# Performance work log

Measured on AMD Instinct MI355X. Metric: run time of the kernel, lower is better.

Reference implementation:

```python
import jax, jax.numpy as jnp
import numpy as np

B, N, E, D, F_IN, EDGE_DIM, VN = 128, 500, 1048576, 128, 5, 2, 10
NEG_FEAT = 0.01   # torch F.leaky_relu default
NEG_ATT = 0.2     # GAT attention slope


def _gat_layer(h_in, src, dst, edge_attr, W, b, a_src, a_dst, a_edge, We, n_nodes):
    # Edge-feature GAT conv: per-edge attention over (src, dst, edge) then
    # softmax-normalized scatter-aggregate onto destination nodes.
    h = h_in @ W                                  # [N, d]
    e = edge_attr @ We                            # [E, d] projected edge features
    logits = jax.nn.leaky_relu((h @ a_src)[src] + (h @ a_dst)[dst] + e @ a_edge,
                               negative_slope=NEG_ATT)    # [E]
    # segment softmax over incoming edges of each dst node
    m = jax.ops.segment_max(logits, dst, num_segments=n_nodes)
    ex = jnp.exp(logits - m[dst])
    denom = jax.ops.segment_sum(ex, dst, num_segments=n_nodes)
    alpha = ex / (denom[dst] + 1e-16)             # [E]
    msg = h[src] + e                              # [E, d]
    out = jax.ops.segment_sum(alpha[:, None] * msg, dst, num_segments=n_nodes)
    return out + b


def setup_inputs() -> dict:
    key = jax.random.key(0)
    ks = jax.random.split(key, 20)
    s = 0.05
    return {
        'x': jax.random.normal(ks[0], (B * N, F_IN), jnp.float32),
        'edge_index': jax.random.randint(ks[1], (2, E), 0, B * N, jnp.int64 if jax.config.jax_enable_x64 else jnp.int32).astype(jnp.int32),
        'edge_attr': jax.random.uniform(ks[2], (E, EDGE_DIM), jnp.float32),
        'curr_v_node_id': jax.random.randint(ks[3], (B,), 0, VN).astype(jnp.int32),
        'v_graph_embedding': jax.random.normal(ks[4], (B, D), jnp.float32),
        'v_node_dense_embeddings': jax.random.normal(ks[5], (B, VN, D), jnp.float32),
        'p_W': jax.random.normal(ks[6], (F_IN, D), jnp.float32) * s,
        'p_b': jnp.zeros((D,), jnp.float32),
        'Ws': jax.random.normal(ks[7], (4, D, D), jnp.float32) * s,
        'bs': jnp.zeros((4, D), jnp.float32),
        'a_srcs': jax.random.normal(ks[8], (4, D), jnp.float32) * s,
        'a_dsts': jax.random.normal(ks[9], (4, D), jnp.float32) * s,
        'a_edges': jax.random.normal(ks[10], (4, D), jnp.float32) * s,
        'Wes': jax.random.normal(ks[11], (4, EDGE_DIM, D), jnp.float32) * s,
        'W5': jax.random.normal(ks[12], (D, 1), jnp.float32) * s,
        'b5': jnp.zeros((1,), jnp.float32),
        'a_src5': jax.random.normal(ks[13], (1,), jnp.float32) * s,
        'a_dst5': jax.random.normal(ks[14], (1,), jnp.float32) * s,
        'a_edge5': jax.random.normal(ks[15], (1,), jnp.float32) * s,
        'We5': jax.random.normal(ks[16], (EDGE_DIM, 1), jnp.float32) * s,
    }


def reference(x, edge_index, edge_attr, curr_v_node_id, v_graph_embedding,
              v_node_dense_embeddings, p_W, p_b, Ws, bs, a_srcs, a_dsts,
              a_edges, Wes, W5, b5, a_src5, a_dst5, a_edge5, We5):
    n_nodes = x.shape[0]
    src, dst = edge_index[0], edge_index[1]
    # gather current v-node embedding: [B, D]
    curr_emb = v_node_dense_embeddings[jnp.arange(B), curr_v_node_id]
    # linear + leaky_relu then broadcast-add of graph/node context
    h = jax.nn.leaky_relu(x @ p_W + p_b, negative_slope=NEG_FEAT)  # [B*N, D]
    h = h.reshape(B, N, D) + v_graph_embedding[:, None, :] + curr_emb[:, None, :]
    h = h.reshape(B * N, D)
    # 4 hidden edge-feature GAT layers (128 -> 128) with leaky_relu
    for l in range(4):
        h = _gat_layer(h, src, dst, edge_attr, Ws[l], bs[l], a_srcs[l],
                       a_dsts[l], a_edges[l], Wes[l], n_nodes)
        h = jax.nn.leaky_relu(h, negative_slope=NEG_FEAT)
    # output layer (128 -> 1), no activation
    h = _gat_layer(h, src, dst, edge_attr, W5, b5, a_src5, a_dst5, a_edge5,
                   We5, n_nodes)                    # [B*N, 1]
    return h.reshape(B, N)
```

## Files before the change

### kernel.cpp

```cpp
#include <hip/hip_runtime.h>
#include <hip/hip_bf16.h>

#define BB   128
#define NN   500
#define NV   64000
#define EE   1048576
#define DD   128
#define FIN  5
#define VNN  10
#define NBUK 250
#define BCAP 8192

typedef unsigned int   uint32;
typedef unsigned short u16b;
typedef __attribute__((ext_vector_type(8))) short short8;
typedef __attribute__((ext_vector_type(4))) float float4v;
typedef __attribute__((ext_vector_type(2))) float float2v;

#define P_ASRC  0
#define P_ADST  512
#define P_WE    1024
#define P_BIAS  2048
#define P_W5    2560
#define P_CVEC  2688
#define P_SC5   2700
#define P_ASD   2816
#define P_TOT   3840

static __device__ __forceinline__ float bf2f(__hip_bfloat16 v) { return __bfloat162float(v); }
static __device__ __forceinline__ float lo2f(uint32 u) { return __uint_as_float(u << 16); }
static __device__ __forceinline__ float hi2f(uint32 u) { return __uint_as_float(u & 0xFFFF0000u); }
static __device__ __forceinline__ uint32 f2bf_bits(float f) {
    uint32 u = __float_as_uint(f);
    return (u + 0x7FFFu + ((u >> 16) & 1u)) >> 16;
}
static __device__ __forceinline__ uint32 pack2(float a, float b) {
    return (f2bf_bits(a) & 0xFFFFu) | (f2bf_bits(b) << 16);
}
static __device__ __forceinline__ float2v unp2(uint32 u) {
    float2v r; r.x = lo2f(u); r.y = hi2f(u); return r;
}
static __device__ __forceinline__ float2v fma2(float2v a, float2v b, float2v c) {
#if __has_builtin(__builtin_elementwise_fma)
    return __builtin_elementwise_fma(a, b, c);
#else
    float2v r; r.x = fmaf(a.x, b.x, c.x); r.y = fmaf(a.y, b.y, c.y); return r;
#endif
}
static __device__ __forceinline__ float2v fma2s(float2v a, float w, float2v c) {
    float2v ww = {w, w};
    return fma2(a, ww, c);
}
static __device__ __forceinline__ float2v shfl_xor2(float2v v, int o) {
    double d; __builtin_memcpy(&d, &v, 8);
    d = __shfl_xor(d, o, 64);
    float2v r; __builtin_memcpy(&r, &d, 8);
    return r;
}
static __device__ __forceinline__ float2v lrelu2(float2v x, float slope) {
    float2v z = {0.f, 0.f};
#if __has_builtin(__builtin_elementwise_max)
    float2v p = __builtin_elementwise_max(x, z);
    float2v q = __builtin_elementwise_min(x, z);
#else
    float2v p; p.x = fmaxf(x.x, 0.f); p.y = fmaxf(x.y, 0.f);
    float2v q; q.x = fminf(x.x, 0.f); q.y = fminf(x.y, 0.f);
#endif
    float2v s = {slope, slope};
    return fma2(q, s, p);
}
static __device__ __forceinline__ float ldf(const void* p, int i, int flag) {
    return flag ? ((const float*)p)[i] : bf2f(((const __hip_bfloat16*)p)[i]);
}

__global__ void sniff_kernel(const unsigned short* __restrict__ p16, int* __restrict__ FLAG) {
    __shared__ int sHigh, sZero;
    if (threadIdx.x == 0) { sHigh = 0; sZero = 0; }
    __syncthreads();
    unsigned short v = p16[2 * threadIdx.x];
    if (v >= 0x8000u) atomicOr(&sHigh, 1);
    if (v == 0)       atomicAdd(&sZero, 1);
    __syncthreads();
    if (threadIdx.x == 0) FLAG[0] = (sHigh || sZero >= 128) ? 1 : 0;
}

__global__ void zero_out_kernel(void* __restrict__ out, const int* __restrict__ FLAG, float tag) {
    int i = blockIdx.x * blockDim.x + threadIdx.x;
    if (i >= NV) return;
    float v = (i == 0) ? tag : 0.f;
    if (FLAG[0]) ((float*)out)[i] = v;
    else         ((u16b*)out)[i] = (u16b)f2bf_bits(v);
}

__global__ void prep_kernel(const void* __restrict__ Wes, const void* __restrict__ aeg,
                            const void* __restrict__ We5, const void* __restrict__ ae5,
                            const void* __restrict__ asr, const void* __restrict__ ads,
                            const void* __restrict__ bs, const void* __restrict__ W5,
                            const void* __restrict__ b5, const void* __restrict__ as5,
                            const void* __restrict__ ad5, const int* __restrict__ FLAG,
                            float* __restrict__ PAR) {
    const int flag = FLAG[0];
    if (blockIdx.x == 0) {
        for (int i = threadIdx.x; i < 512; i += 256) PAR[P_ASRC + i] = ldf(asr, i, flag);
    } else if (blockIdx.x == 1) {
        for (int i = threadIdx.x; i < 512; i += 256) PAR[P_ADST + i] = ldf(ads, i, flag);
    } else if (blockIdx.x == 2) {
        for (int i = threadIdx.x; i < 1024; i += 256) PAR[P_WE + i] = ldf(Wes, i, flag);
    } else if (blockIdx.x == 3) {
        for (int i = threadIdx.x; i < 512; i += 256) PAR[P_BIAS + i] = ldf(bs, i, flag);
    } else if (blockIdx.x == 4) {
        int tid = threadIdx.x;
        if (tid < 128) {
            PAR[P_W5 + tid] = ldf(W5, tid, flag);
        } else if (tid < 136) {
            int l = (tid - 128) >> 1, r = (tid - 128) & 1;
            float s = 0.f;
            for (int ch = 0; ch < DD; ++ch)
                s += ldf(Wes, l * 256 + r * DD + ch, flag) * ldf(aeg, l * DD + ch, flag);
            PAR[P_CVEC + l * 2 + r] = s;
        } else if (tid == 136) {
            float ae = ldf(ae5, 0, flag);
            float w0 = ldf(We5, 0, flag), w1 = ldf(We5, 1, flag);
            PAR[P_CVEC + 8] = w0 * ae; PAR[P_CVEC + 9] = w1 * ae;
            PAR[P_CVEC + 10] = w0;     PAR[P_CVEC + 11] = w1;
            PAR[P_SC5 + 0] = ldf(b5, 0, flag);
            PAR[P_SC5 + 1] = ldf(as5, 0, flag);
            PAR[P_SC5 + 2] = ldf(ad5, 0, flag);
        }
    } else if (blockIdx.x == 5) {
        for (int i = threadIdx.x; i < 512; i += 256) {
            int l = i >> 7, c = i & 127;
            PAR[P_ASD + l * 256 + c * 2]     = ldf(asr, l * DD + c, flag);
            PAR[P_ASD + l * 256 + c * 2 + 1] = ldf(ads, l * DD + c, flag);
        }
    }
}

__global__ __launch_bounds__(256) void prepack_kernel(const void* __restrict__ Ws,
                                                      const int* __restrict__ FLAG,
                                                      u16b* __restrict__ WB) {
    const int flag = FLAG[0];
    int t = blockIdx.x * 256 + threadIdx.x;
    int lane = t & 63;
    int frag = t >> 6;
    int nchunk = frag & 7, kblk = (frag >> 3) & 3, l = frag >> 5;
    int n = nchunk * 16 + (lane & 15);
    int kbase = kblk * 32 + (lane >> 4) * 8;
#pragma unroll
    for (int j = 0; j < 8; ++j) {
        int idx = l * 16384 + (kbase + j) * 128 + n;
        u16b bits = flag ? (u16b)f2bf_bits(((const float*)Ws)[idx])
                         : ((const u16b*)Ws)[idx];
        WB[(size_t)t * 8 + j] = bits;
    }
}

__global__ __launch_bounds__(256) void proj_kernel(
        const void* __restrict__ x, const void* __restrict__ pW,
        const void* __restrict__ pb, const int* __restrict__ curr,
        const void* __restrict__ vge, const void* __restrict__ vnd,
        const int* __restrict__ FLAG, uint32* __restrict__ H) {
    const int flag = FLAG[0];
    const int n = blockIdx.x * 4 + (threadIdx.x >> 6);
    const int lane = threadIdx.x & 63;
    const int b = n / NN;
    int cv = curr[b]; if ((unsigned)cv >= VNN) cv = 0;
    float xv[FIN];
#pragma unroll
    for (int k = 0; k < FIN; ++k) xv[k] = ldf(x, n * FIN + k, flag);
    const int ch = lane * 2;
    float s0 = ldf(pb, ch, flag), s1 = ldf(pb, ch + 1, flag);
#pragma unroll
    for (int k = 0; k < FIN; ++k) {
        s0 = fmaf(xv[k], ldf(pW, k * DD + ch, flag), s0);
        s1 = fmaf(xv[k], ldf(pW, k * DD + ch + 1, flag), s1);
    }
    s0 = (s0 > 0.f) ? s0 : 0.01f * s0;
    s1 = (s1 > 0.f) ? s1 : 0.01f * s1;
    s0 += ldf(vge, b * DD + ch, flag) + ldf(vnd, (b * VNN + cv) * DD + ch, flag);
    s1 += ldf(vge, b * DD + ch + 1, flag) + ldf(vnd, (b * VNN + cv) * DD + ch + 1, flag);
    H[(size_t)n * 64 + lane] = pack2(s0, s1);
}

__global__ void init_kernel(int* __restrict__ gcur, int* __restrict__ counts) {
    int t = blockIdx.x * 256 + threadIdx.x;
    if (t < NBUK) gcur[t] = t * BCAP;
    if (t < 512) counts[NV + t] = 0;
}

__global__ __launch_bounds__(256) void bucketize_kernel(
        const int* __restrict__ src, const int* __restrict__ dst,
        const void* __restrict__ eaP, const int* __restrict__ FLAG,
        int* __restrict__ gcur, uint32* __restrict__ bukx, uint32* __restrict__ buky) {
    __shared__ int cnt[256];
    __shared__ int cur[256];
    const int flag = FLAG[0];
    const int t = threadIdx.x;
    const int e0 = blockIdx.x * 4096;
    cnt[t] = 0;
    __syncthreads();
    int d[16];
#pragma unroll
    for (int i = 0; i < 16; ++i) {
        d[i] = dst[e0 + i * 256 + t];
        if ((unsigned)d[i] >= NV) d[i] = -1;
        if (d[i] >= 0) atomicAdd(&cnt[d[i] >> 8], 1);
    }
    __syncthreads();
    if (t < NBUK) {
        int c = cnt[t];
        cur[t] = c ? atomicAdd(&gcur[t], c) : 0;
    }
    __syncthreads();
#pragma unroll
    for (int i = 0; i < 16; ++i) {
        if (d[i] < 0) continue;
        int e = e0 + i * 256 + t;
        int b = d[i] >> 8;
        int s = src[e];
        if ((unsigned)s >= NV) s = 0;
        uint32 eb;
        if (flag) { float2 v = ((const float2*)eaP)[e]; eb = pack2(v.x, v.y); }
        else      eb = ((const uint32*)eaP)[e];
        int p = atomicAdd(&cur[b], 1);
        if (p < (b + 1) * BCAP) {
            bukx[p] = (uint32)((s & 0xFFFF) | ((d[i] & 255) << 16));
            buky[p] = eb;
        }
    }
}

__global__ __launch_bounds__(256) void bcount_kernel(
        const uint32* __restrict__ bukx, const int* __restrict__ gcur,
        int* __restrict__ counts) {
    __shared__ int c[256];
    const int b = blockIdx.x, t = threadIdx.x;
    c[t] = 0;
    __syncthreads();
    const int base = b * BCAP;
    int cnt = gcur[b] - base;
    if (cnt > BCAP) cnt = BCAP;
    for (int i = t; i < cnt; i += 256)
        atomicAdd(&c[(bukx[base + i] >> 16) & 255], 1);
    __syncthreads();
    counts[b * 256 + t] = c[t];
}

__global__ __launch_bounds__(256) void scan1_kernel(const int* __restrict__ counts,
                                                    int* __restrict__ row_ptr,
                                                    int* __restrict__ partials) {
    __shared__ int sdata[256];
    int tid = threadIdx.x;
    int4 v = ((const int4*)counts)[blockIdx.x * 256 + tid];
    int sum = v.x + v.y + v.z + v.w;
    sdata[tid] = sum;
    __syncthreads();
    int acc = sum;
    for (int off = 1; off < 256; off <<= 1) {
        int t = (tid >= off) ? sdata[tid - off] : 0;
        __syncthreads();
        acc += t;
        sdata[tid] = acc;
        __syncthreads();
    }
    int excl = acc - sum;
    int base = blockIdx.x * 1024 + tid * 4;
    int run = excl;
    if (base + 0 <= NV) row_ptr[base + 0] = run; run += v.x;
    if (base + 1 <= NV) row_ptr[base + 1] = run; run += v.y;
    if (base + 2 <= NV) row_ptr[base + 2] = run; run += v.z;
    if (base + 3 <= NV) row_ptr[base + 3] = run;
    if (tid == 255) partials[blockIdx.x] = acc;
}

__global__ __launch_bounds__(64) void scan2_kernel(const int* __restrict__ partials,
                                                   int* __restrict__ boff, int nb) {
    int lane = threadIdx.x;
    int v = (lane < nb) ? partials[lane] : 0;
    int orig = v;
#pragma unroll
    for (int off = 1; off < 64; off <<= 1) {
        int t = __shfl_up(v, off, 64);
        if (lane >= off) v += t;
    }
    boff[lane] = v - orig;
}

__global__ __launch_bounds__(256) void scan3_kernel(int* __restrict__ row_ptr,
                                                    const int* __restrict__ boff) {
    int add = boff[blockIdx.x];
    int base = blockIdx.x * 1024 + threadIdx.x * 4;
#pragma unroll
    for (int j = 0; j < 4; ++j) {
        int i = base + j;
        if (i <= NV) row_ptr[i] += add;
    }
}

__global__ __launch_bounds__(256) void bscatter_kernel(
        const uint32* __restrict__ bukx, const uint32* __restrict__ buky,
        const int* __restrict__ gcur, const int* __restrict__ row_ptr,
        uint2* __restrict__ csr2) {
    __shared__ int cur[256];
    const int b = blockIdx.x, t = threadIdx.x;
    cur[t] = row_ptr[b * 256 + t];
    __syncthreads();
    const int base = b * BCAP;
    int cnt = gcur[b] - base;
    if (cnt > BCAP) cnt = BCAP;
    for (int i = t; i < cnt; i += 256) {
        uint32 x = bukx[base + i];
        uint32 y = buky[base + i];
        int p = atomicAdd(&cur[(x >> 16) & 255], 1);
        csr2[p] = make_uint2(x & 0xFFFFu, y);
    }
}

__global__ __launch_bounds__(256) void gemm_kernel(
        const uint32* __restrict__ Hu, const u16b* __restrict__ WBl,
        const float* __restrict__ ASDl, uint32* __restrict__ HWu,
        float* __restrict__ ssrc, float* __restrict__ sdst) {
    __shared__ float hs[64 * 129];
    const int tid = threadIdx.x;
    const int lane = tid & 63;
    const int wave = tid >> 6;
    const int quad = lane >> 4;
    const int n0 = blockIdx.x * 64;
    const int m = n0 + wave * 16 + (lane & 15);

    const u16b* hrow = (const u16b*)Hu + (size_t)m * 128;
    short8 a0 = *(const short8*)(hrow + 0  + quad * 8);
    short8 a1 = *(const short8*)(hrow + 32 + quad * 8);
    short8 a2 = *(const short8*)(hrow + 64 + quad * 8);
    short8 a3 = *(const short8*)(hrow + 96 + quad * 8);

    const float2v* asd = (const float2v*)ASDl;
    float2v psd[4];
#pragma unroll
    for (int r = 0; r < 4; ++r) { psd[r].x = 0.f; psd[r].y = 0.f; }

#pragma unroll
    for (int nt = 0; nt < 8; ++nt) {
        const u16b* bbase = WBl + ((size_t)nt * 512 + lane * 8);
        short8 b0 = *(const short8*)(bbase + 0 * 4096);
        short8 b1 = *(const short8*)(bbase + 1 * 4096);
        short8 b2 = *(const short8*)(bbase + 2 * 4096);
        short8 b3 = *(const short8*)(bbase + 3 * 4096);
        float4v acc = {0.f, 0.f, 0.f, 0.f};
        acc = __builtin_amdgcn_mfma_f32_16x16x32_bf16(a0, b0, acc, 0, 0, 0);
        acc = __builtin_amdgcn_mfma_f32_16x16x32_bf16(a1, b1, acc, 0, 0, 0);
        acc = __builtin_amdgcn_mfma_f32_16x16x32_bf16(a2, b2, acc, 0, 0, 0);
        acc = __builtin_amdgcn_mfma_f32_16x16x32_bf16(a3, b3, acc, 0, 0, 0);
        float2v av = asd[nt * 16 + (lane & 15)];
#pragma unroll
        for (int r = 0; r < 4; ++r) {
            hs[(wave * 16 + quad * 4 + r) * 129 + nt * 16 + (lane & 15)] = acc[r];
            psd[r] = fma2s(av, acc[r], psd[r]);
        }
    }
#pragma unroll
    for (int r = 0; r < 4; ++r) {
#pragma unroll
        for (int o = 1; o < 16; o <<= 1) {
            float2v other = shfl_xor2(psd[r], o);
            psd[r].x += other.x; psd[r].y += other.y;
        }
    }
    if ((lane & 15) == 0) {
#pragma unroll
        for (int r = 0; r < 4; ++r) {
            int row = n0 + wave * 16 + quad * 4 + r;
            ssrc[row] = psd[r].x;
            sdst[row] = psd[r].y;
        }
    }
    __syncthreads();

#pragma unroll
    for (int i = 0; i < 4; ++i) {
        int flat = i * 2048 + tid * 8;
        int n = flat >> 7, c = flat & 127;
        const float* p = hs + n * 129 + c;
        uint4 v;
        v.x = pack2(p[0], p[1]); v.y = pack2(p[2], p[3]);
        v.z = pack2(p[4], p[5]); v.w = pack2(p[6], p[7]);
        *(uint4*)(HWu + (size_t)(n0 + n) * 64 + c / 2) = v;
    }
}

__global__ __launch_bounds__(256, 4) void fused_kernel(
        const uint32* __restrict__ HWin, const float* __restrict__ ssrc,
        const float* __restrict__ sdst, const uint2* __restrict__ csr2,
        const int* __restrict__ row_ptr, const float* __restrict__ PAR,
        int layer, const u16b* __restrict__ WBn, const float* __restrict__ ASDn,
        uint32* __restrict__ HWout, float* __restrict__ ssrc_o,
        float* __restrict__ sdst_o, float* __restrict__ hw5out, int wantw5) {
    __shared__ uint32 Hlds[64 * 68];
    __shared__ float exs[4][64];
    const int tid = threadIdx.x;
    const int lane = tid & 63;
    const int wid = tid >> 6;
    const int n0 = blockIdx.x * 64;
    const float c0 = PAR[P_CVEC + 2 * layer], c1 = PAR[P_CVEC + 2 * layer + 1];
    const int ch = lane * 2;
    const float* WEl = PAR + P_WE + layer * 256;
    const float* Bl  = PAR + P_BIAS + layer * DD;
    const float2v we0 = *(const float2v*)(WEl + ch);
    const float2v we1 = *(const float2v*)(WEl + DD + ch);
    const float2v bl  = *(const float2v*)(Bl + ch);
    float w50 = 0.f, w51 = 0.f;
    if (wantw5) { w50 = PAR[P_W5 + ch]; w51 = PAR[P_W5 + ch + 1]; }

    for (int i = 0; i < 16; ++i) {
        const int n = n0 + wid * 16 + i;
        const int begin = __builtin_amdgcn_readfirstlane(row_ptr[n]);
        const int deg   = __builtin_amdgcn_readfirstlane(row_ptr[n + 1]) - begin;
        const float sd = sdst[n];

        int   sv = 0;
        uint32 eb = 0;
        if (lane < deg) {
            uint2 se = csr2[begin + lane];
            sv = (int)se.x;
            eb = se.y;
        }
        const float ssv = ssrc[sv];

        const int dmain = (deg < 64) ? deg : 64;
        const int npad  = (dmain + 15) & ~15;

        uint32 hA[16], hB[16];
#pragma unroll
        for (int q = 0; q < 16; ++q) {
            int s = __builtin_amdgcn_readlane(sv, q);
            hA[q] = HWin[(s << 6) + lane];
        }
        if (npad > 16) {
#pragma unroll
            for (int q = 0; q < 16; ++q) {
                int s = __builtin_amdgcn_readlane(sv, 16 + q);
                hB[q] = HWin[(s << 6) + lane];
            }
        }

        float ex = 0.f;
        if (lane < deg) {
            float L = fmaf(hi2f(eb), c1, fmaf(lo2f(eb), c0, ssv + sd));
            L = (L > 0.f) ? L : 0.2f * L;
            ex = __expf(fminf(L, 60.f));
        }
        exs[wid][lane] = ex;

        float2v acc2 = {0.f, 0.f};
        const float* wp = &exs[wid][0];
#pragma unroll
        for (int q0 = 0; q0 < 16; q0 += 4) {
            float4 w4 = *(const float4*)(wp + q0);
            acc2 = fma2s(unp2(hA[q0 + 0]), w4.x, acc2);
            acc2 = fma2s(unp2(hA[q0 + 1]), w4.y, acc2);
            acc2 = fma2s(unp2(hA[q0 + 2]), w4.z, acc2);
            acc2 = fma2s(unp2(hA[q0 + 3]), w4.w, acc2);
        }
        if (npad > 16) {
#pragma unroll
            for (int q0 = 16; q0 < 32; q0 += 4) {
                float4 w4 = *(const float4*)(wp + q0);
                acc2 = fma2s(unp2(hB[q0 - 16]), w4.x, acc2);
                acc2 = fma2s(unp2(hB[q0 - 15]), w4.y, acc2);
                acc2 = fma2s(unp2(hB[q0 - 14]), w4.z, acc2);
                acc2 = fma2s(unp2(hB[q0 - 13]), w4.w, acc2);
            }
        }
        for (int j = 32; j < dmain; ++j) {
            int s = __builtin_amdgcn_readlane(sv, j);
            float w = wp[j];
            acc2 = fma2s(unp2(HWin[(s << 6) + lane]), w, acc2);
        }

        float dsum = ex;
        float2v sxy = unp2(eb);
        sxy.x *= ex; sxy.y *= ex;
        for (int j0 = 64; j0 < deg; j0 += 64) {
            int j = j0 + lane;
            if (j < deg) {
                uint2 se2 = csr2[begin + j];
                float L2 = fmaf(hi2f(se2.y), c1, fmaf(lo2f(se2.y), c0, ssrc[se2.x] + sd));
                L2 = (L2 > 0.f) ? L2 : 0.2f * L2;
                float x2 = __expf(fminf(L2, 60.f));
                dsum += x2;
                sxy = fma2s(unp2(se2.y), x2, sxy);
            }
        }
#pragma unroll
        for (int o = 32; o; o >>= 1) {
            dsum += __shfl_xor(dsum, o, 64);
            float2v other = shfl_xor2(sxy, o);
            sxy.x += other.x; sxy.y += other.y;
        }

        for (int jj = 64; jj < deg; ++jj) {
            uint2 se2 = csr2[begin + jj];
            float L2 = fmaf(hi2f(se2.y), c1, fmaf(lo2f(se2.y), c0, ssrc[se2.x] + sd));
            L2 = (L2 > 0.f) ? L2 : 0.2f * L2;
            float x2 = __expf(fminf(L2, 60.f));
            acc2 = fma2s(unp2(HWin[(size_t)se2.x * 64 + lane]), x2, acc2);
        }

        const float inv = __builtin_amdgcn_rcpf(dsum + 1e-16f);
        float2v t2 = fma2s(we1, sxy.y, fma2s(we0, sxy.x, acc2));
        float2v o2 = fma2s(t2, inv, bl);
        o2 = lrelu2(o2, 0.01f);

        if (wantw5) {
            float p = o2.x * w50 + o2.y * w51;
#pragma unroll
            for (int o = 32; o; o >>= 1) p += __shfl_xor(p, o, 64);
            if (lane == 0) hw5out[n] = p;
        } else {
            Hlds[(wid * 16 + i) * 68 + lane] = pack2(o2.x, o2.y);
        }
    }
    if (wantw5) return;

    const int quad = lane >> 4;
    const int mloc = wid * 16 + (lane & 15);
    short8 a0 = *(const short8*)(Hlds + mloc * 68 + 0 * 16 + quad * 4);
    short8 a1 = *(const short8*)(Hlds + mloc * 68 + 1 * 16 + quad * 4);
    short8 a2 = *(const short8*)(Hlds + mloc * 68 + 2 * 16 + quad * 4);
    short8 a3 = *(const short8*)(Hlds + mloc * 68 + 3 * 16 + quad * 4);

    const float2v* asd = (const float2v*)ASDn;
    float2v psd[4];
#pragma unroll
    for (int r = 0; r < 4; ++r) { psd[r].x = 0.f; psd[r].y = 0.f; }

#pragma unroll
    for (int nt = 0; nt < 8; ++nt) {
        const u16b* bbase = WBn + ((size_t)nt * 512 + lane * 8);
        short8 b0 = *(const short8*)(bbase + 0 * 4096);
        short8 b1 = *(const short8*)(bbase + 1 * 4096);
        short8 b2 = *(const short8*)(bbase + 2 * 4096);
        short8 b3 = *(const short8*)(bbase + 3 * 4096);
        float4v acc = {0.f, 0.f, 0.f, 0.f};
        acc = __builtin_amdgcn_mfma_f32_16x16x32_bf16(a0, b0, acc, 0, 0, 0);
        acc = __builtin_amdgcn_mfma_f32_16x16x32_bf16(a1, b1, acc, 0, 0, 0);
        acc = __builtin_amdgcn_mfma_f32_16x16x32_bf16(a2, b2, acc, 0, 0, 0);
        acc = __builtin_amdgcn_mfma_f32_16x16x32_bf16(a3, b3, acc, 0, 0, 0);
        float2v av = asd[nt * 16 + (lane & 15)];
#pragma unroll
        for (int r = 0; r < 4; ++r) {
            psd[r] = fma2s(av, acc[r], psd[r]);
            float vn = __shfl_xor(acc[r], 1, 64);
            if (!(lane & 1)) {
                int row = wid * 16 + quad * 4 + r;
                Hlds[row * 68 + nt * 8 + ((lane & 15) >> 1)] = pack2(acc[r], vn);
            }
        }
    }
#pragma unroll
    for (int r = 0; r < 4; ++r) {
#pragma unroll
        for (int o = 1; o < 16; o <<= 1) {
            float2v other = shfl_xor2(psd[r], o);
            psd[r].x += other.x; psd[r].y += other.y;
        }
    }
    if ((lane & 15) == 0) {
#pragma unroll
        for (int r = 0; r < 4; ++r) {
            int row = n0 + wid * 16 + quad * 4 + r;
            ssrc_o[row] = psd[r].x;
            sdst_o[row] = psd[r].y;
        }
    }
    __syncthreads();

#pragma unroll
    for (int j = 0; j < 4; ++j) {
        int flat = j * 1024 + tid * 4;
        int row = flat >> 6, w = flat & 63;
        uint4 v = *(const uint4*)(Hlds + row * 68 + w);
        *(uint4*)(HWout + (size_t)(n0 + row) * 64 + w) = v;
    }
}

__global__ __launch_bounds__(256) void final_kernel(
        const float* __restrict__ hw5, const uint2* __restrict__ csr2,
        const int* __restrict__ row_ptr, const float* __restrict__ PAR,
        const int* __restrict__ FLAG, void* __restrict__ out) {
    const int flag = FLAG[0];
    int lane = threadIdx.x & 63;
    int n = blockIdx.x * 4 + (threadIdx.x >> 6);
    int begin = __builtin_amdgcn_readfirstlane(row_ptr[n]);
    int deg   = __builtin_amdgcn_readfirstlane(row_ptr[n + 1]) - begin;
    float c50 = PAR[P_CVEC + 8], c51 = PAR[P_CVEC + 9];
    float ce0 = PAR[P_CVEC + 10], ce1 = PAR[P_CVEC + 11];
    float b5v = PAR[P_SC5], a5s = PAR[P_SC5 + 1];
    float hd = PAR[P_SC5 + 2] * hw5[n];

    float dsum = 0.f, msum = 0.f;
    for (int j0 = 0; j0 < deg; j0 += 64) {
        int j = j0 + lane;
        if (j < deg) {
            uint2 se = csr2[begin + j];
            float hs5 = hw5[se.x];
            float L = fmaf(hi2f(se.y), c51, fmaf(lo2f(se.y), c50, fmaf(a5s, hs5, hd)));
            L = (L > 0.f) ? L : 0.2f * L;
            float ex = __expf(fminf(L, 60.f));
            dsum += ex;
            msum = fmaf(ex, hs5 + fmaf(hi2f(se.y), ce1, lo2f(se.y) * ce0), msum);
        }
    }
#pragma unroll
    for (int o = 32; o; o >>= 1) {
        dsum += __shfl_xor(dsum, o, 64);
        msum += __shfl_xor(msum, o, 64);
    }
    if (lane == 0) {
        float r = msum * __builtin_amdgcn_rcpf(dsum + 1e-16f) + b5v;
        if (flag) ((float*)out)[n] = r;
        else      ((u16b*)out)[n] = (u16b)f2bf_bits(r);
    }
}

extern "C" void kernel_launch(void* const* d_in, const int* in_sizes, int n_in,
                              void* d_out, int out_size, void* d_ws, size_t ws_size,
                              hipStream_t stream) {
    const void* x   = d_in[0];
    const int*  ei  = (const int*)d_in[1];
    const void* ea  = d_in[2];
    const int*  cur = (const int*)d_in[3];
    const void* vge = d_in[4];
    const void* vnd = d_in[5];
    const void* pW  = d_in[6];
    const void* pb  = d_in[7];
    const void* Ws  = d_in[8];
    const void* bs  = d_in[9];
    const void* asr = d_in[10];
    const void* ads = d_in[11];
    const void* aeg = d_in[12];
    const void* Wes = d_in[13];
    const void* W5  = d_in[14];
    const void* b5  = d_in[15];
    const void* as5 = d_in[16];
    const void* ad5 = d_in[17];
    const void* ae5 = d_in[18];
    const void* We5 = d_in[19];
    (void)in_sizes; (void)n_in; (void)out_size;

    const int* e_src = ei;
    const int* e_dst = ei + EE;

    size_t off = 0;
    char* base = (char*)d_ws;
    auto carve = [&](size_t bytes) {
        void* p = base + off;
        off += (bytes + 255) & ~(size_t)255;
        return p;
    };
    int*    FLAG   = (int*)carve(256);
    float*  PAR    = (float*)carve((size_t)P_TOT * 4);
    u16b*   WB     = (u16b*)carve(4 * DD * DD * 2);
    uint32* H0     = (uint32*)carve((size_t)NV * DD * 2);
    uint32* H1     = (uint32*)carve((size_t)NV * DD * 2);
    float*  SS0    = (float*)carve(NV * 4);
    float*  SD0    = (float*)carve(NV * 4);
    float*  SS1    = (float*)carve(NV * 4);
    float*  SD1    = (float*)carve(NV * 4);
    float*  HW5v   = (float*)carve(NV * 4);
    int*    COUNTS = (int*)carve(65536 * 4);
    int*    ROWPTR = (int*)carve(65536 * 4);
    int*    GCUR   = (int*)carve(256 * 4);
    int*    PART   = (int*)carve(256 * 4);
    int*    BOFF   = (int*)carve(256 * 4);
    uint2*  CSR2   = (uint2*)carve((size_t)EE * 8);
    size_t need = off;

    uint32* BUKX = H1;
    uint32* BUKY = H1 + (size_t)NBUK * BCAP;

    sniff_kernel<<<1, 256, 0, stream>>>((const unsigned short*)ea, FLAG);

    if (need > ws_size) {
        zero_out_kernel<<<(NV + 255) / 256, 256, 0, stream>>>(
            d_out, FLAG, (float)(ws_size >> 20));
        return;
    }

    prep_kernel<<<6, 256, 0, stream>>>(Wes, aeg, We5, ae5, asr, ads, bs,
                                       W5, b5, as5, ad5, FLAG, PAR);
    prepack_kernel<<<32, 256, 0, stream>>>(Ws, FLAG, WB);
    proj_kernel<<<NV / 4, 256, 0, stream>>>(x, pW, pb, cur, vge, vnd, FLAG, H0);

    init_kernel<<<2, 256, 0, stream>>>(GCUR, COUNTS);
    bucketize_kernel<<<EE / 4096, 256, 0, stream>>>(e_src, e_dst, ea, FLAG,
                                                    GCUR, BUKX, BUKY);
    bcount_kernel<<<NBUK, 256, 0, stream>>>(BUKX, GCUR, COUNTS);
    scan1_kernel<<<63, 256, 0, stream>>>(COUNTS, ROWPTR, PART);
    scan2_kernel<<<1, 64, 0, stream>>>(PART, BOFF, 63);
    scan3_kernel<<<63, 256, 0, stream>>>(ROWPTR, BOFF);
    bscatter_kernel<<<NBUK, 256, 0, stream>>>(BUKX, BUKY, GCUR, ROWPTR, CSR2);

    gemm_kernel<<<NV / 64, 256, 0, stream>>>(
        H0, WB, PAR + P_ASD, H1, SS0, SD0);
    fused_kernel<<<NV / 64, 256, 0, stream>>>(
        H1, SS0, SD0, CSR2, ROWPTR, PAR, 0,
        WB + (size_t)1 * 16384, PAR + P_ASD + 1 * 256,
        H0, SS1, SD1, HW5v, 0);
    fused_kernel<<<NV / 64, 256, 0, stream>>>(
        H0, SS1, SD1, CSR2, ROWPTR, PAR, 1,
        WB + (size_t)2 * 16384, PAR + P_ASD + 2 * 256,
        H1, SS0, SD0, HW5v, 0);
    fused_kernel<<<NV / 64, 256, 0, stream>>>(
        H1, SS0, SD0, CSR2, ROWPTR, PAR, 2,
        WB + (size_t)3 * 16384, PAR + P_ASD + 3 * 256,
        H0, SS1, SD1, HW5v, 0);
    fused_kernel<<<NV / 64, 256, 0, stream>>>(
        H0, SS1, SD1, CSR2, ROWPTR, PAR, 3,
        WB, PAR + P_ASD, H1, SS0, SD0, HW5v, 1);

    final_kernel<<<NV / 4, 256, 0, stream>>>(HW5v, CSR2, ROWPTR, PAR,
                                             FLAG, d_out);
}
```

Before: 420.2 us.

## Software-pipeline neighbor gathers across nodes and split CSR into SoA arrays

The fused aggregation kernel now prefetches row pointers four nodes ahead, CSR entries two nodes ahead and the neighbor feature rows one node ahead into double-buffered registers. This overlaps gather latency for the next destination node with the compute for the current one. The interleaved CSR (src, edge attr) array is split into two separate arrays, and the occupancy hint on launch bounds is removed. The row double buffer raises register pressure and may cut occupancy.

```diff
diff --git a/kernel.cpp b/kernel.cpp
--- a/kernel.cpp
+++ b/kernel.cpp
@@ -300,7 +300,7 @@
 __global__ __launch_bounds__(256) void bscatter_kernel(
         const uint32* __restrict__ bukx, const uint32* __restrict__ buky,
         const int* __restrict__ gcur, const int* __restrict__ row_ptr,
-        uint2* __restrict__ csr2) {
+        int* __restrict__ csr_src, uint32* __restrict__ csr_ea) {
     __shared__ int cur[256];
     const int b = blockIdx.x, t = threadIdx.x;
     cur[t] = row_ptr[b * 256 + t];
@@ -312,7 +312,8 @@
         uint32 x = bukx[base + i];
         uint32 y = buky[base + i];
         int p = atomicAdd(&cur[(x >> 16) & 255], 1);
-        csr2[p] = make_uint2(x & 0xFFFFu, y);
+        csr_src[p] = (int)(x & 0xFFFFu);
+        csr_ea[p]  = y;
     }
 }
 
@@ -388,19 +389,21 @@
     }
 }
 
-__global__ __launch_bounds__(256, 4) void fused_kernel(
+__global__ __launch_bounds__(256) void fused_kernel(
         const uint32* __restrict__ HWin, const float* __restrict__ ssrc,
-        const float* __restrict__ sdst, const uint2* __restrict__ csr2,
-        const int* __restrict__ row_ptr, const float* __restrict__ PAR,
-        int layer, const u16b* __restrict__ WBn, const float* __restrict__ ASDn,
+        const float* __restrict__ sdst, const int* __restrict__ csr_src,
+        const uint32* __restrict__ csr_ea, const int* __restrict__ row_ptr,
+        const float* __restrict__ PAR, int layer,
+        const u16b* __restrict__ WBn, const float* __restrict__ ASDn,
         uint32* __restrict__ HWout, float* __restrict__ ssrc_o,
         float* __restrict__ sdst_o, float* __restrict__ hw5out, int wantw5) {
     __shared__ uint32 Hlds[64 * 68];
-    __shared__ float exs[4][64];
+    __shared__ float exs[4][2][64];
     const int tid = threadIdx.x;
     const int lane = tid & 63;
     const int wid = tid >> 6;
     const int n0 = blockIdx.x * 64;
+    const int nbase = n0 + wid * 16;
     const float c0 = PAR[P_CVEC + 2 * layer], c1 = PAR[P_CVEC + 2 * layer + 1];
     const int ch = lane * 2;
     const float* WEl = PAR + P_WE + layer * 256;
@@ -411,64 +414,103 @@
     float w50 = 0.f, w51 = 0.f;
     if (wantw5) { w50 = PAR[P_W5 + ch]; w51 = PAR[P_W5 + ch + 1]; }
 
+    float sdv = (lane < 16) ? sdst[nbase + lane] : 0.f;
+
+    int b4[4];
+    b4[0] = __builtin_amdgcn_readfirstlane(row_ptr[nbase + 0]);
+    b4[1] = __builtin_amdgcn_readfirstlane(row_ptr[nbase + 1]);
+    b4[2] = __builtin_amdgcn_readfirstlane(row_ptr[nbase + 2]);
+    b4[3] = __builtin_amdgcn_readfirstlane(row_ptr[nbase + 3]);
+
+    int   svp[4] = {0, 0, 0, 0};
+    uint32 ebp[4] = {0, 0, 0, 0};
+    float ssvp[2];
+    uint32 rows[2][32];
+
+    {
+        int dg0 = b4[1] - b4[0];
+        if (lane < dg0) { svp[0] = csr_src[b4[0] + lane]; ebp[0] = csr_ea[b4[0] + lane]; }
+        int dg1 = b4[2] - b4[1];
+        if (lane < dg1) { svp[1] = csr_src[b4[1] + lane]; ebp[1] = csr_ea[b4[1] + lane]; }
+        ssvp[0] = ssrc[svp[0]];
+        int dm0 = (dg0 < 64) ? dg0 : 64;
+        int np0 = (dm0 + 15) & ~15;
+#pragma unroll
+        for (int q = 0; q < 16; ++q)
+            rows[0][q] = HWin[(__builtin_amdgcn_readlane(svp[0], q) << 6) + lane];
+        if (np0 > 16) {
+#pragma unroll
+            for (int q = 0; q < 16; ++q)
+                rows[0][16 + q] = HWin[(__builtin_amdgcn_readlane(svp[0], 16 + q) << 6) + lane];
+        }
+    }
+
+#pragma unroll 4
     for (int i = 0; i < 16; ++i) {
-        const int n = n0 + wid * 16 + i;
-        const int begin = __builtin_amdgcn_readfirstlane(row_ptr[n]);
-        const int deg   = __builtin_amdgcn_readfirstlane(row_ptr[n + 1]) - begin;
-        const float sd = sdst[n];
-
-        int   sv = 0;
-        uint32 eb = 0;
-        if (lane < deg) {
-            uint2 se = csr2[begin + lane];
-            sv = (int)se.x;
-            eb = se.y;
-        }
-        const float ssv = ssrc[sv];
-
+        const int begin = b4[i & 3];
+        const int deg   = b4[(i + 1) & 3] - begin;
+        const int beg1  = b4[(i + 1) & 3];
+        const int beg2  = b4[(i + 2) & 3];
+        const int beg3  = b4[(i + 3) & 3];
+        {
+            int nx = (i + 4 <= 16) ? (i + 4) : 16;
+            b4[i & 3] = __builtin_amdgcn_readfirstlane(row_ptr[nbase + nx]);
+        }
+        if (i + 2 < 16) {
+            int dg2 = beg3 - beg2;
+            int s2 = 0; uint32 e2 = 0;
+            if (lane < dg2) { s2 = csr_src[beg2 + lane]; e2 = csr_ea[beg2 + lane]; }
+            svp[(i + 2) & 3] = s2; ebp[(i + 2) & 3] = e2;
+        }
+        if (i + 1 < 16) {
+            int sv1 = svp[(i + 1) & 3];
+            ssvp[(i + 1) & 1] = ssrc[sv1];
+            int dg1 = beg2 - beg1;
+            int dm1 = (dg1 < 64) ? dg1 : 64;
+            int np1 = (dm1 + 15) & ~15;
+#pragma unroll
+            for (int q = 0; q < 16; ++q)
+                rows[(i + 1) & 1][q] = HWin[(__builtin_amdgcn_readlane(sv1, q) << 6) + lane];
+            if (np1 > 16) {
+#pragma unroll
+                for (int q = 0; q < 16; ++q)
+                    rows[(i + 1) & 1][16 + q] = HWin[(__builtin_amdgcn_readlane(sv1, 16 + q) << 6) + lane];
+            }
+        }
+
+        const float sd = __uint_as_float(
+            __builtin_amdgcn_readlane((int)__float_as_uint(sdv), i));
+        const int   sv = svp[i & 3];
+        const uint32 eb = ebp[i & 3];
         const int dmain = (deg < 64) ? deg : 64;
         const int npad  = (dmain + 15) & ~15;
 
-        uint32 hA[16], hB[16];
-#pragma unroll
-        for (int q = 0; q < 16; ++q) {
-            int s = __builtin_amdgcn_readlane(sv, q);
-            hA[q] = HWin[(s << 6) + lane];
-        }
-        if (npad > 16) {
-#pragma unroll
-            for (int q = 0; q < 16; ++q) {
-                int s = __builtin_amdgcn_readlane(sv, 16 + q);
-                hB[q] = HWin[(s << 6) + lane];
-            }
-        }
-
         float ex = 0.f;
         if (lane < deg) {
-            float L = fmaf(hi2f(eb), c1, fmaf(lo2f(eb), c0, ssv + sd));
+            float L = fmaf(hi2f(eb), c1, fmaf(lo2f(eb), c0, ssvp[i & 1] + sd));
             L = (L > 0.f) ? L : 0.2f * L;
             ex = __expf(fminf(L, 60.f));
         }
-        exs[wid][lane] = ex;
+        exs[wid][i & 1][lane] = ex;
 
         float2v acc2 = {0.f, 0.f};
-        const float* wp = &exs[wid][0];
+        const float* wp = &exs[wid][i & 1][0];
 #pragma unroll
         for (int q0 = 0; q0 < 16; q0 += 4) {
             float4 w4 = *(const float4*)(wp + q0);
-            acc2 = fma2s(unp2(hA[q0 + 0]), w4.x, acc2);
-            acc2 = fma2s(unp2(hA[q0 + 1]), w4.y, acc2);
-            acc2 = fma2s(unp2(hA[q0 + 2]), w4.z, acc2);
-            acc2 = fma2s(unp2(hA[q0 + 3]), w4.w, acc2);
+            acc2 = fma2s(unp2(rows[i & 1][q0 + 0]), w4.x, acc2);
+            acc2 = fma2s(unp2(rows[i & 1][q0 + 1]), w4.y, acc2);
+            acc2 = fma2s(unp2(rows[i & 1][q0 + 2]), w4.z, acc2);
+            acc2 = fma2s(unp2(rows[i & 1][q0 + 3]), w4.w, acc2);
         }
         if (npad > 16) {
 #pragma unroll
             for (int q0 = 16; q0 < 32; q0 += 4) {
                 float4 w4 = *(const float4*)(wp + q0);
-                acc2 = fma2s(unp2(hB[q0 - 16]), w4.x, acc2);
-                acc2 = fma2s(unp2(hB[q0 - 15]), w4.y, acc2);
-                acc2 = fma2s(unp2(hB[q0 - 14]), w4.z, acc2);
-                acc2 = fma2s(unp2(hB[q0 - 13]), w4.w, acc2);
+                acc2 = fma2s(unp2(rows[i & 1][q0 + 0]), w4.x, acc2);
+                acc2 = fma2s(unp2(rows[i & 1][q0 + 1]), w4.y, acc2);
+                acc2 = fma2s(unp2(rows[i & 1][q0 + 2]), w4.z, acc2);
+                acc2 = fma2s(unp2(rows[i & 1][q0 + 3]), w4.w, acc2);
             }
         }
         for (int j = 32; j < dmain; ++j) {
@@ -483,12 +525,13 @@
         for (int j0 = 64; j0 < deg; j0 += 64) {
             int j = j0 + lane;
             if (j < deg) {
-                uint2 se2 = csr2[begin + j];
-                float L2 = fmaf(hi2f(se2.y), c1, fmaf(lo2f(se2.y), c0, ssrc[se2.x] + sd));
+                int s2 = csr_src[begin + j];
+                uint32 e2 = csr_ea[begin + j];
+                float L2 = fmaf(hi2f(e2), c1, fmaf(lo2f(e2), c0, ssrc[s2] + sd));
                 L2 = (L2 > 0.f) ? L2 : 0.2f * L2;
                 float x2 = __expf(fminf(L2, 60.f));
                 dsum += x2;
-                sxy = fma2s(unp2(se2.y), x2, sxy);
+                sxy = fma2s(unp2(e2), x2, sxy);
             }
         }
 #pragma unroll
@@ -497,13 +540,13 @@
             float2v other = shfl_xor2(sxy, o);
             sxy.x += other.x; sxy.y += other.y;
         }
-
         for (int jj = 64; jj < deg; ++jj) {
-            uint2 se2 = csr2[begin + jj];
-            float L2 = fmaf(hi2f(se2.y), c1, fmaf(lo2f(se2.y), c0, ssrc[se2.x] + sd));
+            int s = csr_src[begin + jj];
+            uint32 e2 = csr_ea[begin + jj];
+            float L2 = fmaf(hi2f(e2), c1, fmaf(lo2f(e2), c0, ssrc[s] + sd));
             L2 = (L2 > 0.f) ? L2 : 0.2f * L2;
             float x2 = __expf(fminf(L2, 60.f));
-            acc2 = fma2s(unp2(HWin[(size_t)se2.x * 64 + lane]), x2, acc2);
+            acc2 = fma2s(unp2(HWin[(size_t)s * 64 + lane]), x2, acc2);
         }
 
         const float inv = __builtin_amdgcn_rcpf(dsum + 1e-16f);
@@ -515,7 +558,7 @@
             float p = o2.x * w50 + o2.y * w51;
 #pragma unroll
             for (int o = 32; o; o >>= 1) p += __shfl_xor(p, o, 64);
-            if (lane == 0) hw5out[n] = p;
+            if (lane == 0) hw5out[nbase + i] = p;
         } else {
             Hlds[(wid * 16 + i) * 68 + lane] = pack2(o2.x, o2.y);
         }
@@ -585,9 +628,10 @@
 }
 
 __global__ __launch_bounds__(256) void final_kernel(
-        const float* __restrict__ hw5, const uint2* __restrict__ csr2,
-        const int* __restrict__ row_ptr, const float* __restrict__ PAR,
-        const int* __restrict__ FLAG, void* __restrict__ out) {
+        const float* __restrict__ hw5, const int* __restrict__ csr_src,
+        const uint32* __restrict__ csr_ea, const int* __restrict__ row_ptr,
+        const float* __restrict__ PAR, const int* __restrict__ FLAG,
+        void* __restrict__ out) {
     const int flag = FLAG[0];
     int lane = threadIdx.x & 63;
     int n = blockIdx.x * 4 + (threadIdx.x >> 6);
@@ -602,13 +646,14 @@
     for (int j0 = 0; j0 < deg; j0 += 64) {
         int j = j0 + lane;
         if (j < deg) {
-            uint2 se = csr2[begin + j];
-            float hs5 = hw5[se.x];
-            float L = fmaf(hi2f(se.y), c51, fmaf(lo2f(se.y), c50, fmaf(a5s, hs5, hd)));
+            int s = csr_src[begin + j];
+            uint32 eb = csr_ea[begin + j];
+            float hs5 = hw5[s];
+            float L = fmaf(hi2f(eb), c51, fmaf(lo2f(eb), c50, fmaf(a5s, hs5, hd)));
             L = (L > 0.f) ? L : 0.2f * L;
             float ex = __expf(fminf(L, 60.f));
             dsum += ex;
-            msum = fmaf(ex, hs5 + fmaf(hi2f(se.y), ce1, lo2f(se.y) * ce0), msum);
+            msum = fmaf(ex, hs5 + fmaf(hi2f(eb), ce1, lo2f(eb) * ce0), msum);
         }
     }
 #pragma unroll
@@ -673,7 +718,8 @@
     int*    GCUR   = (int*)carve(256 * 4);
     int*    PART   = (int*)carve(256 * 4);
     int*    BOFF   = (int*)carve(256 * 4);
-    uint2*  CSR2   = (uint2*)carve((size_t)EE * 8);
+    int*    CSRS   = (int*)carve((size_t)EE * 4);
+    uint32* CSREA  = (uint32*)carve((size_t)EE * 4);
     size_t need = off;
 
     uint32* BUKX = H1;
@@ -699,26 +745,27 @@
     scan1_kernel<<<63, 256, 0, stream>>>(COUNTS, ROWPTR, PART);
     scan2_kernel<<<1, 64, 0, stream>>>(PART, BOFF, 63);
     scan3_kernel<<<63, 256, 0, stream>>>(ROWPTR, BOFF);
-    bscatter_kernel<<<NBUK, 256, 0, stream>>>(BUKX, BUKY, GCUR, ROWPTR, CSR2);
+    bscatter_kernel<<<NBUK, 256, 0, stream>>>(BUKX, BUKY, GCUR, ROWPTR,
+                                              CSRS, CSREA);
 
     gemm_kernel<<<NV / 64, 256, 0, stream>>>(
         H0, WB, PAR + P_ASD, H1, SS0, SD0);
     fused_kernel<<<NV / 64, 256, 0, stream>>>(
-        H1, SS0, SD0, CSR2, ROWPTR, PAR, 0,
+        H1, SS0, SD0, CSRS, CSREA, ROWPTR, PAR, 0,
         WB + (size_t)1 * 16384, PAR + P_ASD + 1 * 256,
         H0, SS1, SD1, HW5v, 0);
     fused_kernel<<<NV / 64, 256, 0, stream>>>(
-        H0, SS1, SD1, CSR2, ROWPTR, PAR, 1,
+        H0, SS1, SD1, CSRS, CSREA, ROWPTR, PAR, 1,
         WB + (size_t)2 * 16384, PAR + P_ASD + 2 * 256,
         H1, SS0, SD0, HW5v, 0);
     fused_kernel<<<NV / 64, 256, 0, stream>>>(
-        H1, SS0, SD0, CSR2, ROWPTR, PAR, 2,
+        H1, SS0, SD0, CSRS, CSREA, ROWPTR, PAR, 2,
         WB + (size_t)3 * 16384, PAR + P_ASD + 3 * 256,
         H0, SS1, SD1, HW5v, 0);
     fused_kernel<<<NV / 64, 256, 0, stream>>>(
-        H0, SS1, SD1, CSR2, ROWPTR, PAR, 3,
+        H0, SS1, SD1, CSRS, CSREA, ROWPTR, PAR, 3,
         WB, PAR + P_ASD, H1, SS0, SD0, HW5v, 1);
 
-    final_kernel<<<NV / 4, 256, 0, stream>>>(HW5v, CSR2, ROWPTR, PAR,
+    final_kernel<<<NV / 4, 256, 0, stream>>>(HW5v, CSRS, CSREA, ROWPTR, PAR,
                                              FLAG, d_out);
 }
```

New measurement: 454.0 us. 1.08x slower.

## Shrink fused GAT block to 16 nodes and split MFMA N-tiles across waves

Applied to the files above, without the earlier changes.

Each fused-layer block now handles 16 destination nodes instead of 64, so 4x more blocks are launched. Each wave aggregates 4 nodes, and the following 16x128 GEMM is split so each wave computes 2 of the 8 N-tiles for all 16 rows. Partial attention-score sums are reduced across waves through a small shared buffer. The aim is better load balance over the irregular degree distribution and lower LDS use per block, at the cost of extra block barriers and reloading the weight tiles in more blocks. The occupancy hint in launch_bounds is dropped.

```diff
diff --git a/kernel.cpp b/kernel.cpp
--- a/kernel.cpp
+++ b/kernel.cpp
@@ -388,19 +388,20 @@
     }
 }
 
-__global__ __launch_bounds__(256, 4) void fused_kernel(
+__global__ __launch_bounds__(256) void fused_kernel(
         const uint32* __restrict__ HWin, const float* __restrict__ ssrc,
         const float* __restrict__ sdst, const uint2* __restrict__ csr2,
         const int* __restrict__ row_ptr, const float* __restrict__ PAR,
         int layer, const u16b* __restrict__ WBn, const float* __restrict__ ASDn,
         uint32* __restrict__ HWout, float* __restrict__ ssrc_o,
         float* __restrict__ sdst_o, float* __restrict__ hw5out, int wantw5) {
-    __shared__ uint32 Hlds[64 * 68];
+    __shared__ uint32 Hlds[16 * 68];
     __shared__ float exs[4][64];
+    __shared__ float2 pp[4][16];
     const int tid = threadIdx.x;
     const int lane = tid & 63;
     const int wid = tid >> 6;
-    const int n0 = blockIdx.x * 64;
+    const int n0 = blockIdx.x * 16;
     const float c0 = PAR[P_CVEC + 2 * layer], c1 = PAR[P_CVEC + 2 * layer + 1];
     const int ch = lane * 2;
     const float* WEl = PAR + P_WE + layer * 256;
@@ -411,8 +412,9 @@
     float w50 = 0.f, w51 = 0.f;
     if (wantw5) { w50 = PAR[P_W5 + ch]; w51 = PAR[P_W5 + ch + 1]; }
 
-    for (int i = 0; i < 16; ++i) {
-        const int n = n0 + wid * 16 + i;
+#pragma unroll 1
+    for (int j = 0; j < 4; ++j) {
+        const int n = n0 + wid * 4 + j;
         const int begin = __builtin_amdgcn_readfirstlane(row_ptr[n]);
         const int deg   = __builtin_amdgcn_readfirstlane(row_ptr[n + 1]) - begin;
         const float sd = sdst[n];
@@ -471,9 +473,9 @@
                 acc2 = fma2s(unp2(hB[q0 - 13]), w4.w, acc2);
             }
         }
-        for (int j = 32; j < dmain; ++j) {
-            int s = __builtin_amdgcn_readlane(sv, j);
-            float w = wp[j];
+        for (int jj = 32; jj < dmain; ++jj) {
+            int s = __builtin_amdgcn_readlane(sv, jj);
+            float w = wp[jj];
             acc2 = fma2s(unp2(HWin[(s << 6) + lane]), w, acc2);
         }
 
@@ -481,9 +483,9 @@
         float2v sxy = unp2(eb);
         sxy.x *= ex; sxy.y *= ex;
         for (int j0 = 64; j0 < deg; j0 += 64) {
-            int j = j0 + lane;
-            if (j < deg) {
-                uint2 se2 = csr2[begin + j];
+            int jj = j0 + lane;
+            if (jj < deg) {
+                uint2 se2 = csr2[begin + jj];
                 float L2 = fmaf(hi2f(se2.y), c1, fmaf(lo2f(se2.y), c0, ssrc[se2.x] + sd));
                 L2 = (L2 > 0.f) ? L2 : 0.2f * L2;
                 float x2 = __expf(fminf(L2, 60.f));
@@ -497,7 +499,6 @@
             float2v other = shfl_xor2(sxy, o);
             sxy.x += other.x; sxy.y += other.y;
         }
-
         for (int jj = 64; jj < deg; ++jj) {
             uint2 se2 = csr2[begin + jj];
             float L2 = fmaf(hi2f(se2.y), c1, fmaf(lo2f(se2.y), c0, ssrc[se2.x] + sd));
@@ -517,17 +518,19 @@
             for (int o = 32; o; o >>= 1) p += __shfl_xor(p, o, 64);
             if (lane == 0) hw5out[n] = p;
         } else {
-            Hlds[(wid * 16 + i) * 68 + lane] = pack2(o2.x, o2.y);
+            Hlds[(wid * 4 + j) * 68 + lane] = pack2(o2.x, o2.y);
         }
     }
     if (wantw5) return;
+    __syncthreads();
 
     const int quad = lane >> 4;
-    const int mloc = wid * 16 + (lane & 15);
-    short8 a0 = *(const short8*)(Hlds + mloc * 68 + 0 * 16 + quad * 4);
-    short8 a1 = *(const short8*)(Hlds + mloc * 68 + 1 * 16 + quad * 4);
-    short8 a2 = *(const short8*)(Hlds + mloc * 68 + 2 * 16 + quad * 4);
-    short8 a3 = *(const short8*)(Hlds + mloc * 68 + 3 * 16 + quad * 4);
+    const int m = lane & 15;
+    short8 a0 = *(const short8*)(Hlds + m * 68 + 0 * 16 + quad * 4);
+    short8 a1 = *(const short8*)(Hlds + m * 68 + 1 * 16 + quad * 4);
+    short8 a2 = *(const short8*)(Hlds + m * 68 + 2 * 16 + quad * 4);
+    short8 a3 = *(const short8*)(Hlds + m * 68 + 3 * 16 + quad * 4);
+    __syncthreads();
 
     const float2v* asd = (const float2v*)ASDn;
     float2v psd[4];
@@ -535,7 +538,8 @@
     for (int r = 0; r < 4; ++r) { psd[r].x = 0.f; psd[r].y = 0.f; }
 
 #pragma unroll
-    for (int nt = 0; nt < 8; ++nt) {
+    for (int t = 0; t < 2; ++t) {
+        const int nt = wid * 2 + t;
         const u16b* bbase = WBn + ((size_t)nt * 512 + lane * 8);
         short8 b0 = *(const short8*)(bbase + 0 * 4096);
         short8 b1 = *(const short8*)(bbase + 1 * 4096);
@@ -546,14 +550,13 @@
         acc = __builtin_amdgcn_mfma_f32_16x16x32_bf16(a1, b1, acc, 0, 0, 0);
         acc = __builtin_amdgcn_mfma_f32_16x16x32_bf16(a2, b2, acc, 0, 0, 0);
         acc = __builtin_amdgcn_mfma_f32_16x16x32_bf16(a3, b3, acc, 0, 0, 0);
-        float2v av = asd[nt * 16 + (lane & 15)];
+        float2v av = asd[nt * 16 + m];
 #pragma unroll
         for (int r = 0; r < 4; ++r) {
             psd[r] = fma2s(av, acc[r], psd[r]);
             float vn = __shfl_xor(acc[r], 1, 64);
             if (!(lane & 1)) {
-                int row = wid * 16 + quad * 4 + r;
-                Hlds[row * 68 + nt * 8 + ((lane & 15) >> 1)] = pack2(acc[r], vn);
+                Hlds[(quad * 4 + r) * 68 + nt * 8 + (m >> 1)] = pack2(acc[r], vn);
             }
         }
     }
@@ -565,22 +568,23 @@
             psd[r].x += other.x; psd[r].y += other.y;
         }
     }
-    if ((lane & 15) == 0) {
-#pragma unroll
-        for (int r = 0; r < 4; ++r) {
-            int row = n0 + wid * 16 + quad * 4 + r;
-            ssrc_o[row] = psd[r].x;
-            sdst_o[row] = psd[r].y;
-        }
-    }
-    __syncthreads();
-
-#pragma unroll
-    for (int j = 0; j < 4; ++j) {
-        int flat = j * 1024 + tid * 4;
-        int row = flat >> 6, w = flat & 63;
+    if (m == 0) {
+#pragma unroll
+        for (int r = 0; r < 4; ++r)
+            pp[wid][quad * 4 + r] = make_float2(psd[r].x, psd[r].y);
+    }
+    __syncthreads();
+
+    {
+        int row = tid >> 4;
+        int w = (tid & 15) * 4;
         uint4 v = *(const uint4*)(Hlds + row * 68 + w);
         *(uint4*)(HWout + (size_t)(n0 + row) * 64 + w) = v;
+    }
+    if (tid < 16) {
+        float2 pa = pp[0][tid], pb = pp[1][tid], pc = pp[2][tid], pd = pp[3][tid];
+        ssrc_o[n0 + tid] = pa.x + pb.x + pc.x + pd.x;
+        sdst_o[n0 + tid] = pa.y + pb.y + pc.y + pd.y;
     }
 }
 
@@ -703,19 +707,19 @@
 
     gemm_kernel<<<NV / 64, 256, 0, stream>>>(
         H0, WB, PAR + P_ASD, H1, SS0, SD0);
-    fused_kernel<<<NV / 64, 256, 0, stream>>>(
+    fused_kernel<<<NV / 16, 256, 0, stream>>>(
         H1, SS0, SD0, CSR2, ROWPTR, PAR, 0,
         WB + (size_t)1 * 16384, PAR + P_ASD + 1 * 256,
         H0, SS1, SD1, HW5v, 0);
-    fused_kernel<<<NV / 64, 256, 0, stream>>>(
+    fused_kernel<<<NV / 16, 256, 0, stream>>>(
         H0, SS1, SD1, CSR2, ROWPTR, PAR, 1,
         WB + (size_t)2 * 16384, PAR + P_ASD + 2 * 256,
         H1, SS0, SD0, HW5v, 0);
-    fused_kernel<<<NV / 64, 256, 0, stream>>>(
+    fused_kernel<<<NV / 16, 256, 0, stream>>>(
         H1, SS0, SD0, CSR2, ROWPTR, PAR, 2,
         WB + (size_t)3 * 16384, PAR + P_ASD + 3 * 256,
         H0, SS1, SD1, HW5v, 0);
-    fused_kernel<<<NV / 64, 256, 0, stream>>>(
+    fused_kernel<<<NV / 16, 256, 0, stream>>>(
         H0, SS1, SD1, CSR2, ROWPTR, PAR, 3,
         WB, PAR + P_ASD, H1, SS0, SD0, HW5v, 1);
 
```

New measurement: 431.3 us. 1.03x slower.
